# Optimization experiments

Measured on AMD Instinct MI355X. Metric: run time of the kernel, lower is better.

## Reference

```python
import jax, jax.numpy as jnp
import numpy as np

V, E, HD, NT = 50001, 256, 512, 24   # vocab, embed_dim, hidden_dim, tag_size
H = HD // 2                          # per-direction LSTM hidden
B, S = 64, 512


def setup_inputs() -> dict:
    key = jax.random.key(0)
    ks = jax.random.split(key, 18)
    lw = lambda k, sh, s=0.05: (jax.random.normal(k, sh, jnp.float32) * s)
    x = jax.random.randint(ks[0], (B, S), 0, V).astype(jnp.int32)
    lengths = jax.random.randint(ks[1], (B,), S // 2, S + 1)
    mask = jnp.arange(S)[None, :] < lengths[:, None]  # [B,S] bool, mask[:,0]=True
    return {
        "x": x,
        "mask": mask,
        "emb": lw(ks[2], (V, E), 0.1),
        "Wih_f": lw(ks[3], (4 * H, E)), "Whh_f": lw(ks[4], (4 * H, H)),
        "bih_f": lw(ks[5], (4 * H,)), "bhh_f": lw(ks[6], (4 * H,)),
        "Wih_b": lw(ks[7], (4 * H, E)), "Whh_b": lw(ks[8], (4 * H, H)),
        "bih_b": lw(ks[9], (4 * H,)), "bhh_b": lw(ks[10], (4 * H,)),
        "Wout": lw(ks[11], (NT, HD)), "bout": lw(ks[12], (NT,)),
        "trans": lw(ks[13], (NT, NT), 0.1),
        "start": lw(ks[14], (NT,), 0.1),
        "end": lw(ks[15], (NT,), 0.1),
    }


def _lstm_dir(xs, Wih, Whh, bih, bhh):
    # xs: [S, B, E] -> hs: [S, B, H]; torch gate order i, f, g, o
    Bn = xs.shape[1]
    h0 = jnp.zeros((Bn, H), xs.dtype)

    def step(carry, xt):
        h, c = carry
        g = xt @ Wih.T + h @ Whh.T + bih + bhh
        i, f, gg, o = jnp.split(g, 4, axis=-1)
        c = jax.nn.sigmoid(f) * c + jax.nn.sigmoid(i) * jnp.tanh(gg)
        h = jax.nn.sigmoid(o) * jnp.tanh(c)
        return (h, c), h

    _, hs = jax.lax.scan(step, (h0, h0), xs)
    return hs


def _viterbi(emissions, mask, trans, start, end):
    # emissions: [B, S, T]; mask: [B, S] bool. Returns (tags [B,S] int, best_score [B]).
    em = emissions.transpose(1, 0, 2)   # [S, B, T]
    mk = mask.transpose(1, 0)           # [S, B]
    nT = trans.shape[0]
    idx_id = jnp.arange(nT)[None, :]    # identity backpointers for padded steps
    score = start[None, :] + em[0]      # [B, T]

    def step(score, inp):
        e_t, m_t = inp
        cand = score[:, :, None] + trans[None, :, :] + e_t[:, None, :]  # [B,Tprev,Tnext]
        idx = jnp.argmax(cand, axis=1)
        best = jnp.max(cand, axis=1)
        idx = jnp.where(m_t[:, None], idx, idx_id)
        new_score = jnp.where(m_t[:, None], best, score)
        return new_score, idx

    score, hist = jax.lax.scan(step, score, (em[1:], mk[1:]))  # hist: [S-1, B, T]
    final = score + end[None, :]
    last_tag = jnp.argmax(final, axis=1)   # [B]
    best_score = jnp.max(final, axis=1)    # [B]

    def back(tag, h_t):
        prev = jnp.take_along_axis(h_t, tag[:, None], axis=1)[:, 0]
        return prev, tag

    tag0, ys = jax.lax.scan(back, last_tag, hist, reverse=True)
    tags = jnp.concatenate([tag0[None, :], ys], axis=0).T  # [B, S]
    return tags, best_score


def reference(x, mask, emb, Wih_f, Whh_f, bih_f, bhh_f, Wih_b, Whh_b, bih_b, bhh_b,
              Wout, bout, trans, start, end):
    e = emb[x]                      # [B, S, E] embedding gather
    xs = e.transpose(1, 0, 2)       # [S, B, E] time-major for scan
    hf = _lstm_dir(xs, Wih_f, Whh_f, bih_f, bhh_f)
    hb = jnp.flip(_lstm_dir(jnp.flip(xs, 0), Wih_b, Whh_b, bih_b, bhh_b), 0)
    h = jnp.concatenate([hf, hb], axis=-1)          # [S, B, HD]
    emis = (h @ Wout.T + bout).transpose(1, 0, 2)   # [B, S, T]
    tags, _ = _viterbi(emis, mask, trans, start, end)
    return tags
```

## Files before the change

### kernel.cpp

```cpp
#include <hip/hip_runtime.h>
#include <math.h>

#define B_   64
#define S_   512
#define E_   256
#define H_   256
#define G4H_ 1024
#define NT_  24

static const size_t HBUF_OFF  = 0;
static const size_t CST_OFF   = 131072;
static const size_t WHI_OFF   = 163840;
static const size_t WLO_OFF   = 425984;
static const size_t EMF_OFF   = 688128;
static const size_t EMB_OFF   = 1474560;
static const size_t HOUT_OFF  = 2260992;

typedef short  bf16x8_ __attribute__((ext_vector_type(8)));
typedef float  f32x4_  __attribute__((ext_vector_type(4)));

__device__ __forceinline__ float sigmoidf_(float x) {
  return 1.0f / (1.0f + expf(-x));
}

__device__ __forceinline__ unsigned short bf16_rne_(float v) {
  unsigned u = __float_as_uint(v);
  unsigned r = u + 0x7fffu + ((u >> 16) & 1u);
  return (unsigned short)(r >> 16);
}

__global__ __launch_bounds__(256) void k0_wconv(
    const float* __restrict__ Wf, const float* __restrict__ Wb,
    unsigned short* __restrict__ whi, unsigned short* __restrict__ wlo)
{
  int idx = blockIdx.x * 256 + threadIdx.x;
  int d   = idx >> 16;
  int i4  = idx & 65535;
  const float* W = d ? Wb : Wf;
  float4 v = *(const float4*)(W + (size_t)i4 * 4);
  float vv[4] = {v.x, v.y, v.z, v.w};
  unsigned short h[4], l[4];
#pragma unroll
  for (int e = 0; e < 4; ++e) {
    h[e] = bf16_rne_(vv[e]);
    float hf = __uint_as_float((unsigned)h[e] << 16);
    l[e] = bf16_rne_(vv[e] - hf);
  }
  size_t o = (size_t)d * 262144 + (size_t)i4 * 4;
  whi[o + 0] = h[0]; whi[o + 1] = h[1]; whi[o + 2] = h[2]; whi[o + 3] = h[3];
  wlo[o + 0] = l[0]; wlo[o + 1] = l[1]; wlo[o + 2] = l[2]; wlo[o + 3] = l[3];
}

__global__ __launch_bounds__(256) void k1_xpre_mfma(
    const int* __restrict__ x, const float* __restrict__ emb,
    const unsigned short* __restrict__ whi,
    const unsigned short* __restrict__ wlo,
    const float* __restrict__ bih_f, const float* __restrict__ bhh_f,
    const float* __restrict__ bih_b, const float* __restrict__ bhh_b,
    float* __restrict__ xpre_c, int chunk, int tc)
{
  __shared__ unsigned short Ahi[128][40], Alo[128][40];
  __shared__ unsigned short Bhi[128][40], Blo[128][40];
  __shared__ int xt[128];

  const int tid = threadIdx.x;
  const int wg  = blockIdx.x;
  const int per_dir = 4 * tc;
  const int d   = wg / per_dir;
  const int rem = wg % per_dir;
  const int m0  = (rem >> 3) * 128;
  const int n0  = (rem & 7) * 128;
  const int t0  = chunk * tc;

  const float* bih = d ? bih_b : bih_f;
  const float* bhh = d ? bhh_b : bhh_f;
  const unsigned short* Whi = whi + (size_t)d * 262144;
  const unsigned short* Wlo = wlo + (size_t)d * 262144;

  if (tid < 128) {
    int m = m0 + tid;
    int lt = m >> 6, b = m & 63;
    int tok = d ? (S_ - 1 - (t0 + lt)) : (t0 + lt);
    xt[tid] = x[b * S_ + tok];
  }

  const int lane = tid & 63, wid = tid >> 6;
  const int wr = wid >> 1, wc = wid & 1;
  const int fr = lane & 15, fq = lane >> 4;
  const int sr = tid >> 1, sh = tid & 1;

  f32x4_ acc[4][4];
#pragma unroll
  for (int i = 0; i < 4; ++i)
#pragma unroll
    for (int j = 0; j < 4; ++j) acc[i][j] = (f32x4_){0.f, 0.f, 0.f, 0.f};

  for (int slab = 0; slab < 8; ++slab) {
    const int k0 = slab * 32;
    __syncthreads();
    {
      const float* src = emb + (size_t)xt[sr] * E_ + k0 + sh * 16;
      unsigned short h[16], l[16];
#pragma unroll
      for (int q = 0; q < 4; ++q) {
        float4 v = *(const float4*)(src + q * 4);
        float vv[4] = {v.x, v.y, v.z, v.w};
#pragma unroll
        for (int e = 0; e < 4; ++e) {
          h[q * 4 + e] = bf16_rne_(vv[e]);
          float hf = __uint_as_float((unsigned)h[q * 4 + e] << 16);
          l[q * 4 + e] = bf16_rne_(vv[e] - hf);
        }
      }
      *(bf16x8_*)&Ahi[sr][sh * 16 + 0] = *(bf16x8_*)&h[0];
      *(bf16x8_*)&Ahi[sr][sh * 16 + 8] = *(bf16x8_*)&h[8];
      *(bf16x8_*)&Alo[sr][sh * 16 + 0] = *(bf16x8_*)&l[0];
      *(bf16x8_*)&Alo[sr][sh * 16 + 8] = *(bf16x8_*)&l[8];
    }
    {
      const size_t o = (size_t)(n0 + sr) * E_ + k0 + sh * 16;
      *(bf16x8_*)&Bhi[sr][sh * 16 + 0] = *(const bf16x8_*)(Whi + o);
      *(bf16x8_*)&Bhi[sr][sh * 16 + 8] = *(const bf16x8_*)(Whi + o + 8);
      *(bf16x8_*)&Blo[sr][sh * 16 + 0] = *(const bf16x8_*)(Wlo + o);
      *(bf16x8_*)&Blo[sr][sh * 16 + 8] = *(const bf16x8_*)(Wlo + o + 8);
    }
    __syncthreads();

    bf16x8_ ah[4], al[4], bh[4], bl[4];
#pragma unroll
    for (int mi = 0; mi < 4; ++mi) {
      int row = 64 * wr + mi * 16 + fr;
      ah[mi] = *(bf16x8_*)&Ahi[row][fq * 8];
      al[mi] = *(bf16x8_*)&Alo[row][fq * 8];
    }
#pragma unroll
    for (int ni = 0; ni < 4; ++ni) {
      int row = 64 * wc + ni * 16 + fr;
      bh[ni] = *(bf16x8_*)&Bhi[row][fq * 8];
      bl[ni] = *(bf16x8_*)&Blo[row][fq * 8];
    }
#pragma unroll
    for (int mi = 0; mi < 4; ++mi)
#pragma unroll
      for (int ni = 0; ni < 4; ++ni) {
        acc[mi][ni] = __builtin_amdgcn_mfma_f32_16x16x32_bf16(
            al[mi], bl[ni], acc[mi][ni], 0, 0, 0);
        acc[mi][ni] = __builtin_amdgcn_mfma_f32_16x16x32_bf16(
            al[mi], bh[ni], acc[mi][ni], 0, 0, 0);
        acc[mi][ni] = __builtin_amdgcn_mfma_f32_16x16x32_bf16(
            ah[mi], bl[ni], acc[mi][ni], 0, 0, 0);
        acc[mi][ni] = __builtin_amdgcn_mfma_f32_16x16x32_bf16(
            ah[mi], bh[ni], acc[mi][ni], 0, 0, 0);
      }
  }

  float bias[4];
#pragma unroll
  for (int ni = 0; ni < 4; ++ni) {
    int col = n0 + 64 * wc + ni * 16 + fr;
    bias[ni] = bih[col] + bhh[col];
  }
  const size_t base = (size_t)(d * tc * 64) * G4H_;
#pragma unroll
  for (int mi = 0; mi < 4; ++mi)
#pragma unroll
    for (int ni = 0; ni < 4; ++ni) {
      int col = n0 + 64 * wc + ni * 16 + fr;
#pragma unroll
      for (int r = 0; r < 4; ++r) {
        int m = m0 + 64 * wr + mi * 16 + fq * 4 + r;
        xpre_c[base + (size_t)m * G4H_ + col] = acc[mi][ni][r] + bias[ni];
      }
    }
}

__global__ __launch_bounds__(256, 1) void k2_lstm(
    const float* __restrict__ Whh_f, const float* __restrict__ Whh_b,
    const float* __restrict__ xpre_c, float* __restrict__ hout_c,
    unsigned long long* hbuf, float* cstate, int chunk, int tc)
{
  __shared__ float hTb[16][260];
  __shared__ float part[2][4][16][36];

  const int tid = threadIdx.x;
  const int wg  = blockIdx.x;
  const int d   = wg >> 7;
  const int bg  = (wg >> 5) & 3;
  const int s   = wg & 31;
  const int b0  = bg * 16;
  const float* Whh = d ? Whh_b : Whh_f;

  const int w     = tid >> 6;
  const int lane  = tid & 63;
  const int bl16  = lane & 15;
  const int kb    = lane >> 4;
  const int kbase = w * 64 + kb * 16;
  const int ks    = tid >> 5;
  const int tl    = tid & 31, bt = tl & 3, rt = tl >> 2;
  const int pbl   = tid >> 3, pj = tid & 7;

  float wreg[4][32];
#pragma unroll
  for (int ri = 0; ri < 4; ++ri) {
    int r = rt * 4 + ri, g = r >> 3, j = r & 7;
    const float* src = Whh + ((size_t)(g * H_ + s * 8 + j)) * H_ + ks * 32;
#pragma unroll
    for (int q = 0; q < 8; ++q) {
      float4 v = *(const float4*)(src + q * 4);
      wreg[ri][q * 4 + 0] = v.x; wreg[ri][q * 4 + 1] = v.y;
      wreg[ri][q * 4 + 2] = v.z; wreg[ri][q * 4 + 3] = v.w;
    }
  }

  float c_reg = 0.0f;
  if (chunk > 0 && tid < 128)
    c_reg = cstate[((size_t)d * B_ + b0 + pbl) * H_ + s * 8 + pj];

  for (int tt = 1; tt <= tc; ++tt) {
    const int t  = chunk * tc + tt;
    const int lt = tt - 1;
    const int p  = tt & 1;

    float xp[4];
    if (tid < 128) {
#pragma unroll
      for (int g = 0; g < 4; ++g)
        xp[g] = xpre_c[((size_t)(d * tc + lt) * B_ + b0 + pbl) * G4H_ +
                       g * H_ + s * 8 + pj];
    }

    {
      const unsigned expt = (unsigned)(t - 1);
      const unsigned long long* hb =
          hbuf + ((size_t)(((t - 1) & 1) * 2 + d)) * (256 * 64);
      const size_t a0 = (size_t)kbase * 64 + b0 + bl16;
      unsigned long long e[16];
#pragma unroll
      for (int i = 0; i < 16; ++i)
        e[i] = __hip_atomic_load(hb + a0 + (size_t)i * 64,
                                 __ATOMIC_RELAXED, __HIP_MEMORY_SCOPE_AGENT);
      int lim = 0;
      while (true) {
        unsigned bad = 0;
#pragma unroll
        for (int i = 0; i < 16; ++i)
          if ((unsigned)(e[i] >> 32) != expt) bad |= (1u << i);
        if (bad == 0) break;
        if (++lim > (1 << 18)) break;
#pragma unroll
        for (int i = 0; i < 16; ++i)
          if (bad & (1u << i))
            e[i] = __hip_atomic_load(hb + a0 + (size_t)i * 64,
                                     __ATOMIC_RELAXED,
                                     __HIP_MEMORY_SCOPE_AGENT);
      }
      float4 v0, v1, v2, v3;
      v0.x = __uint_as_float((unsigned)e[0]);  v0.y = __uint_as_float((unsigned)e[1]);
      v0.z = __uint_as_float((unsigned)e[2]);  v0.w = __uint_as_float((unsigned)e[3]);
      v1.x = __uint_as_float((unsigned)e[4]);  v1.y = __uint_as_float((unsigned)e[5]);
      v1.z = __uint_as_float((unsigned)e[6]);  v1.w = __uint_as_float((unsigned)e[7]);
      v2.x = __uint_as_float((unsigned)e[8]);  v2.y = __uint_as_float((unsigned)e[9]);
      v2.z = __uint_as_float((unsigned)e[10]); v2.w = __uint_as_float((unsigned)e[11]);
      v3.x = __uint_as_float((unsigned)e[12]); v3.y = __uint_as_float((unsigned)e[13]);
      v3.z = __uint_as_float((unsigned)e[14]); v3.w = __uint_as_float((unsigned)e[15]);
      *(float4*)&hTb[bl16][kbase +  0] = v0;
      *(float4*)&hTb[bl16][kbase +  4] = v1;
      *(float4*)&hTb[bl16][kbase +  8] = v2;
      *(float4*)&hTb[bl16][kbase + 12] = v3;
    }

    float acc[4][4];
#pragma unroll
    for (int bi = 0; bi < 4; ++bi)
#pragma unroll
      for (int ri = 0; ri < 4; ++ri) acc[bi][ri] = 0.0f;
#pragma unroll
    for (int kq = 0; kq < 8; ++kq) {
      const int k0 = ks * 32 + kq * 4;
      float4 h4[4];
#pragma unroll
      for (int bi = 0; bi < 4; ++bi)
        h4[bi] = *(float4*)&hTb[bt * 4 + bi][k0];
#pragma unroll
      for (int kk = 0; kk < 4; ++kk) {
#pragma unroll
        for (int bi = 0; bi < 4; ++bi) {
          const float hv = kk == 0 ? h4[bi].x : kk == 1 ? h4[bi].y
                         : kk == 2 ? h4[bi].z : h4[bi].w;
#pragma unroll
          for (int ri = 0; ri < 4; ++ri)
            acc[bi][ri] = fmaf(hv, wreg[ri][kq * 4 + kk], acc[bi][ri]);
        }
      }
    }
#pragma unroll
    for (int bi = 0; bi < 4; ++bi)
#pragma unroll
      for (int ri = 0; ri < 4; ++ri)
        acc[bi][ri] += __shfl_xor(acc[bi][ri], 32, 64);
    if (lane < 32) {
#pragma unroll
      for (int bi = 0; bi < 4; ++bi) {
        float4 v = make_float4(acc[bi][0], acc[bi][1], acc[bi][2], acc[bi][3]);
        *(float4*)&part[p][w][bt * 4 + bi][rt * 4] = v;
      }
    }
    __syncthreads();

    if (tid < 128) {
      const int bglob = b0 + pbl;
      float gsum[4];
#pragma unroll
      for (int g = 0; g < 4; ++g) {
        const int r = g * 8 + pj;
        gsum[g] = xp[g] + ((part[p][0][pbl][r] + part[p][1][pbl][r]) +
                           (part[p][2][pbl][r] + part[p][3][pbl][r]));
      }
      float si = sigmoidf_(gsum[0]);
      float sf = sigmoidf_(gsum[1]);
      float tg = tanhf(gsum[2]);
      float so = sigmoidf_(gsum[3]);
      c_reg = sf * c_reg + si * tg;
      float h = so * tanhf(c_reg);
      unsigned long long pk =
          (((unsigned long long)(unsigned)t) << 32) |
          (unsigned long long)__float_as_uint(h);
      __hip_atomic_store(hbuf + ((size_t)((t & 1) * 2 + d)) * (256 * 64) +
                             (size_t)(s * 8 + pj) * 64 + bglob,
                         pk, __ATOMIC_RELAXED, __HIP_MEMORY_SCOPE_AGENT);
      hout_c[((size_t)(d * tc + lt) * B_ + bglob) * H_ + s * 8 + pj] = h;
    }
  }

  if (tid < 128)
    cstate[((size_t)d * B_ + b0 + pbl) * H_ + s * 8 + pj] = c_reg;
}

__global__ __launch_bounds__(256) void k3_emis(
    const float* __restrict__ hout_c, const float* __restrict__ Wout,
    float* __restrict__ emisF, float* __restrict__ emisB, int chunk, int tc)
{
  __shared__ float hh[8][264];
  const int tid = threadIdx.x;
  const int nt8 = tc >> 3;
  const int per_d = 64 * nt8;
  const int d   = blockIdx.x / per_d;
  const int rem = blockIdx.x % per_d;
  const int b   = rem / nt8;
  const int lt0 = (rem % nt8) * 8;
  float* emisX = d ? emisB : emisF;
  {
    int r = tid >> 5, q = tid & 31;
    const float* src = hout_c + ((size_t)(d * tc + lt0 + r) * B_ + b) * H_;
#pragma unroll
    for (int i = 0; i < 2; ++i) {
      int f4i = q + 32 * i;
      *(float4*)&hh[r][f4i * 4] = *(const float4*)(src + f4i * 4);
    }
  }
  __syncthreads();
  if (tid < 192) {
    int r = tid / 24, tag = tid % 24;
    float acc = 0.0f;
    const float* w = Wout + (size_t)tag * 512 + d * 256;
#pragma unroll 4
    for (int k4 = 0; k4 < 64; ++k4) {
      float4 wv = *(const float4*)(w + k4 * 4);
      float4 hv = *(const float4*)&hh[r][k4 * 4];
      acc = fmaf(wv.x, hv.x, acc);
      acc = fmaf(wv.y, hv.y, acc);
      acc = fmaf(wv.z, hv.z, acc);
      acc = fmaf(wv.w, hv.w, acc);
    }
    int lt = lt0 + r;
    int tok = d ? (S_ - 1 - (chunk * tc + lt)) : (chunk * tc + lt);
    emisX[((size_t)b * S_ + tok) * NT_ + tag] = acc;
  }
}

__global__ __launch_bounds__(64) void k4_viterbi(
    const float* __restrict__ emisF, const float* __restrict__ emisB,
    const float* __restrict__ bout, const unsigned char* __restrict__ mb,
    const float* __restrict__ trans, const float* __restrict__ startv,
    const float* __restrict__ endv, int* __restrict__ outp)
{
  __shared__ float tl[24 * 25];
  __shared__ float sc[24];
  __shared__ float fin[24];
  __shared__ unsigned char hist[511 * 24];
  const int b = blockIdx.x;
  const int tid = threadIdx.x;
  const int is_bool = mb[1];

  for (int i = tid; i < 576; i += 64) tl[(i / 24) * 25 + (i % 24)] = trans[i];
  if (tid < 24) {
    size_t e0 = (size_t)b * S_ * NT_ + tid;
    sc[tid] = startv[tid] + (emisF[e0] + emisB[e0] + bout[tid]);
  }
  __syncthreads();

  for (int t = 1; t < S_; ++t) {
    float best = -3.4e38f, scj = 0.f;
    int idx = 0;
    int m;
    {
      int mi = b * S_ + t;
      m = is_bool ? (int)mb[mi] : (int)mb[mi << 2];
    }
    if (tid < 24) {
      size_t ei = ((size_t)b * S_ + t) * NT_ + tid;
      float e = emisF[ei] + emisB[ei] + bout[tid];
      for (int i = 0; i < 24; ++i) {
        float v = (sc[i] + tl[i * 25 + tid]) + e;
        if (v > best) { best = v; idx = i; }
      }
      scj = sc[tid];
    }
    __syncthreads();
    if (tid < 24) {
      sc[tid] = m ? best : scj;
      hist[(t - 1) * 24 + tid] = (unsigned char)(m ? idx : tid);
    }
    __syncthreads();
  }
  if (tid < 24) fin[tid] = sc[tid] + endv[tid];
  __syncthreads();
  if (tid == 0) {
    int tag = 0; float best = fin[0];
    for (int i = 1; i < 24; ++i)
      if (fin[i] > best) { best = fin[i]; tag = i; }
    outp[b * S_ + (S_ - 1)] = tag;
    for (int tt = S_ - 2; tt >= 0; --tt) {
      tag = hist[tt * 24 + tag];
      outp[b * S_ + tt] = tag;
    }
  }
}

extern "C" void kernel_launch(void* const* d_in, const int* in_sizes, int n_in,
                              void* d_out, int out_size, void* d_ws,
                              size_t ws_size, hipStream_t stream)
{
  const int*   x      = (const int*)d_in[0];
  const unsigned char* maskb = (const unsigned char*)d_in[1];
  const float* emb    = (const float*)d_in[2];
  const float* Wih_f  = (const float*)d_in[3];
  const float* Whh_f  = (const float*)d_in[4];
  const float* bih_f  = (const float*)d_in[5];
  const float* bhh_f  = (const float*)d_in[6];
  const float* Wih_b  = (const float*)d_in[7];
  const float* Whh_b  = (const float*)d_in[8];
  const float* bih_b  = (const float*)d_in[9];
  const float* bhh_b  = (const float*)d_in[10];
  const float* Wout   = (const float*)d_in[11];
  const float* bout   = (const float*)d_in[12];
  const float* trans  = (const float*)d_in[13];
  const float* startv = (const float*)d_in[14];
  const float* endv   = (const float*)d_in[15];

  int tc = 8;
  {
    const int cand[6] = {512, 256, 128, 64, 32, 16};
    for (int i = 0; i < 6; ++i) {
      size_t needF = HOUT_OFF + (size_t)cand[i] * (2 * B_ * H_ + 2 * B_ * G4H_);
      if (needF * sizeof(float) <= ws_size) { tc = cand[i]; break; }
    }
  }
  const int nc = S_ / tc;

  float* ws     = (float*)d_ws;
  unsigned long long* hbuf = (unsigned long long*)(ws + HBUF_OFF);
  float* cstate = ws + CST_OFF;
  unsigned short* whi = (unsigned short*)(ws + WHI_OFF);
  unsigned short* wlo = (unsigned short*)(ws + WLO_OFF);
  float* emisF  = ws + EMF_OFF;
  float* emisB  = ws + EMB_OFF;
  float* hout_c = ws + HOUT_OFF;
  float* xpre_c = hout_c + (size_t)tc * 2 * B_ * H_;

  hipMemsetAsync(d_ws, 0, 131072 * sizeof(float), stream);
  hipLaunchKernelGGL(k0_wconv, dim3(512), dim3(256), 0, stream,
                     Wih_f, Wih_b, whi, wlo);

  for (int c = 0; c < nc; ++c) {
    hipLaunchKernelGGL(k1_xpre_mfma, dim3(8 * tc), dim3(256), 0, stream,
                       x, emb, whi, wlo, bih_f, bhh_f, bih_b, bhh_b,
                       xpre_c, c, tc);
    hipLaunchKernelGGL(k2_lstm, dim3(256), dim3(256), 0, stream,
                       Whh_f, Whh_b, xpre_c, hout_c, hbuf, cstate, c, tc);
    hipLaunchKernelGGL(k3_emis, dim3(2 * 64 * (tc / 8)), dim3(256), 0, stream,
                       hout_c, Wout, emisF, emisB, c, tc);
  }
  hipLaunchKernelGGL(k4_viterbi, dim3(64), dim3(64), 0, stream,
                     emisF, emisB, bout, maskb, trans, startv, endv,
                     (int*)d_out);
}
```

Baseline: 2.660 ms.

## Retile LSTM recurrent matvec per thread and preload Viterbi emissions into LDS

The recurrent LSTM kernel now gives each thread 8 batch rows by 4 gate rows over a 16-wide k slice instead of 4x4 over 32. This halves the weight registers and adds a second cross-lane shuffle reduction. The h tile rows are permuted so each thread's batch rows interleave, to reduce LDS bank conflicts. The Viterbi kernel stages the summed forward and backward emissions and the mask into shared memory up front, which takes global-memory latency out of the serial 511-step loop at the cost of about 49KB of extra LDS per block.

```diff
diff --git a/kernel.cpp b/kernel.cpp
--- a/kernel.cpp
+++ b/kernel.cpp
@@ -195,17 +195,19 @@
   const int bl16  = lane & 15;
   const int kb    = lane >> 4;
   const int kbase = w * 64 + kb * 16;
-  const int ks    = tid >> 5;
-  const int tl    = tid & 31, bt = tl & 3, rt = tl >> 2;
+  const int prow  = ((bl16 & 7) << 1) | (bl16 >> 3);
+  const int ksc16 = (tid >> 4) * 16;
+  const int rt    = (tid >> 1) & 7;
+  const int bt    = tid & 1;
   const int pbl   = tid >> 3, pj = tid & 7;
 
-  float wreg[4][32];
+  float wreg[4][16];
 #pragma unroll
   for (int ri = 0; ri < 4; ++ri) {
     int r = rt * 4 + ri, g = r >> 3, j = r & 7;
-    const float* src = Whh + ((size_t)(g * H_ + s * 8 + j)) * H_ + ks * 32;
-#pragma unroll
-    for (int q = 0; q < 8; ++q) {
+    const float* src = Whh + ((size_t)(g * H_ + s * 8 + j)) * H_ + ksc16;
+#pragma unroll
+    for (int q = 0; q < 4; ++q) {
       float4 v = *(const float4*)(src + q * 4);
       wreg[ri][q * 4 + 0] = v.x; wreg[ri][q * 4 + 1] = v.y;
       wreg[ri][q * 4 + 2] = v.z; wreg[ri][q * 4 + 3] = v.w;
@@ -263,28 +265,28 @@
       v2.z = __uint_as_float((unsigned)e[10]); v2.w = __uint_as_float((unsigned)e[11]);
       v3.x = __uint_as_float((unsigned)e[12]); v3.y = __uint_as_float((unsigned)e[13]);
       v3.z = __uint_as_float((unsigned)e[14]); v3.w = __uint_as_float((unsigned)e[15]);
-      *(float4*)&hTb[bl16][kbase +  0] = v0;
-      *(float4*)&hTb[bl16][kbase +  4] = v1;
-      *(float4*)&hTb[bl16][kbase +  8] = v2;
-      *(float4*)&hTb[bl16][kbase + 12] = v3;
-    }
-
-    float acc[4][4];
-#pragma unroll
-    for (int bi = 0; bi < 4; ++bi)
+      *(float4*)&hTb[prow][kbase +  0] = v0;
+      *(float4*)&hTb[prow][kbase +  4] = v1;
+      *(float4*)&hTb[prow][kbase +  8] = v2;
+      *(float4*)&hTb[prow][kbase + 12] = v3;
+    }
+
+    float acc[8][4];
+#pragma unroll
+    for (int bi = 0; bi < 8; ++bi)
 #pragma unroll
       for (int ri = 0; ri < 4; ++ri) acc[bi][ri] = 0.0f;
 #pragma unroll
-    for (int kq = 0; kq < 8; ++kq) {
-      const int k0 = ks * 32 + kq * 4;
-      float4 h4[4];
-#pragma unroll
-      for (int bi = 0; bi < 4; ++bi)
-        h4[bi] = *(float4*)&hTb[bt * 4 + bi][k0];
+    for (int kq = 0; kq < 4; ++kq) {
+      const int k0 = ksc16 + kq * 4;
+      float4 h4[8];
+#pragma unroll
+      for (int bi = 0; bi < 8; ++bi)
+        h4[bi] = *(float4*)&hTb[(bi << 1) | bt][k0];
 #pragma unroll
       for (int kk = 0; kk < 4; ++kk) {
 #pragma unroll
-        for (int bi = 0; bi < 4; ++bi) {
+        for (int bi = 0; bi < 8; ++bi) {
           const float hv = kk == 0 ? h4[bi].x : kk == 1 ? h4[bi].y
                          : kk == 2 ? h4[bi].z : h4[bi].w;
 #pragma unroll
@@ -294,15 +296,17 @@
       }
     }
 #pragma unroll
-    for (int bi = 0; bi < 4; ++bi)
-#pragma unroll
-      for (int ri = 0; ri < 4; ++ri)
+    for (int bi = 0; bi < 8; ++bi)
+#pragma unroll
+      for (int ri = 0; ri < 4; ++ri) {
+        acc[bi][ri] += __shfl_xor(acc[bi][ri], 16, 64);
         acc[bi][ri] += __shfl_xor(acc[bi][ri], 32, 64);
-    if (lane < 32) {
-#pragma unroll
-      for (int bi = 0; bi < 4; ++bi) {
+      }
+    if ((lane & 48) == 0) {
+#pragma unroll
+      for (int bi = 0; bi < 8; ++bi) {
         float4 v = make_float4(acc[bi][0], acc[bi][1], acc[bi][2], acc[bi][3]);
-        *(float4*)&part[p][w][bt * 4 + bi][rt * 4] = v;
+        *(float4*)&part[p][w][bt * 8 + bi][rt * 4] = v;
       }
     }
     __syncthreads();
@@ -385,6 +389,8 @@
     const float* __restrict__ endv, int* __restrict__ outp)
 {
   __shared__ float tl[24 * 25];
+  __shared__ __align__(16) float et[512][24];
+  __shared__ unsigned char mk[512];
   __shared__ float sc[24];
   __shared__ float fin[24];
   __shared__ unsigned char hist[511 * 24];
@@ -393,23 +399,31 @@
   const int is_bool = mb[1];
 
   for (int i = tid; i < 576; i += 64) tl[(i / 24) * 25 + (i % 24)] = trans[i];
-  if (tid < 24) {
-    size_t e0 = (size_t)b * S_ * NT_ + tid;
-    sc[tid] = startv[tid] + (emisF[e0] + emisB[e0] + bout[tid]);
-  }
+  for (int t = tid; t < S_; t += 64) {
+    int mi = b * S_ + t;
+    mk[t] = is_bool ? mb[mi] : mb[mi << 2];
+  }
+  {
+    const float4* eF = (const float4*)(emisF + (size_t)b * S_ * NT_);
+    const float4* eB = (const float4*)(emisB + (size_t)b * S_ * NT_);
+    float4* ed = (float4*)&et[0][0];
+    for (int i = tid; i < (S_ * NT_) / 4; i += 64) {
+      float4 a = eF[i], c = eB[i];
+      ed[i] = make_float4(a.x + c.x, a.y + c.y, a.z + c.z, a.w + c.w);
+    }
+  }
+  const float boutr = (tid < 24) ? bout[tid] : 0.0f;
+  __syncthreads();
+
+  if (tid < 24) sc[tid] = startv[tid] + (et[0][tid] + boutr);
   __syncthreads();
 
   for (int t = 1; t < S_; ++t) {
     float best = -3.4e38f, scj = 0.f;
     int idx = 0;
-    int m;
-    {
-      int mi = b * S_ + t;
-      m = is_bool ? (int)mb[mi] : (int)mb[mi << 2];
-    }
+    const int m = mk[t];
     if (tid < 24) {
-      size_t ei = ((size_t)b * S_ + t) * NT_ + tid;
-      float e = emisF[ei] + emisB[ei] + bout[tid];
+      float e = et[t][tid] + boutr;
       for (int i = 0; i < 24; ++i) {
         float v = (sc[i] + tl[i * 25 + tid]) + e;
         if (v > best) { best = v; idx = i; }
```

After: 2.907 ms. +9.3%, slower.

## Replace per-element tagged h exchange with per-block flags; stage Viterbi emissions in LDS

Applied to the files above, without the earlier changes.

The LSTM recurrence previously packed each h value with a timestep tag into 64-bit words and spun on all of them. It now stores plain floats in a batch-major buffer, and each workgroup raises a release flag after a block barrier. Consumers spin on 32 flags with a wave ballot, then read h with contiguous 64-bit loads. This cuts the polling traffic and the exchanged bytes, at the cost of an extra __syncthreads and a relaxed-acquire ordering subtlety. The Viterbi kernel also preloads the summed emissions and the mask into shared memory, so the serial loop no longer reads global memory.

```diff
diff --git a/kernel.cpp b/kernel.cpp
--- a/kernel.cpp
+++ b/kernel.cpp
@@ -9,6 +9,7 @@
 #define NT_  24
 
 static const size_t HBUF_OFF  = 0;
+static const size_t FLG_OFF   = 65536;
 static const size_t CST_OFF   = 131072;
 static const size_t WHI_OFF   = 163840;
 static const size_t WLO_OFF   = 425984;
@@ -177,7 +178,7 @@
 __global__ __launch_bounds__(256, 1) void k2_lstm(
     const float* __restrict__ Whh_f, const float* __restrict__ Whh_b,
     const float* __restrict__ xpre_c, float* __restrict__ hout_c,
-    unsigned long long* hbuf, float* cstate, int chunk, int tc)
+    float* hbuf2, unsigned* flags, float* cstate, int chunk, int tc)
 {
   __shared__ float hTb[16][260];
   __shared__ float part[2][4][16][36];
@@ -193,8 +194,7 @@
   const int w     = tid >> 6;
   const int lane  = tid & 63;
   const int bl16  = lane & 15;
-  const int kb    = lane >> 4;
-  const int kbase = w * 64 + kb * 16;
+  const int kg    = w * 4 + (lane >> 4);
   const int ks    = tid >> 5;
   const int tl    = tid & 31, bt = tl & 3, rt = tl >> 2;
   const int pbl   = tid >> 3, pj = tid & 7;
@@ -231,42 +231,39 @@
 
     {
       const unsigned expt = (unsigned)(t - 1);
-      const unsigned long long* hb =
-          hbuf + ((size_t)(((t - 1) & 1) * 2 + d)) * (256 * 64);
-      const size_t a0 = (size_t)kbase * 64 + b0 + bl16;
-      unsigned long long e[16];
-#pragma unroll
-      for (int i = 0; i < 16; ++i)
-        e[i] = __hip_atomic_load(hb + a0 + (size_t)i * 64,
-                                 __ATOMIC_RELAXED, __HIP_MEMORY_SCOPE_AGENT);
+      const unsigned* fl =
+          flags + (size_t)((((t - 1) & 1) * 2 + d) * 4 + bg) * 32;
+      unsigned v = expt;
+      if (lane < 32)
+        v = __hip_atomic_load(fl + lane, __ATOMIC_RELAXED,
+                              __HIP_MEMORY_SCOPE_AGENT);
       int lim = 0;
-      while (true) {
-        unsigned bad = 0;
-#pragma unroll
-        for (int i = 0; i < 16; ++i)
-          if ((unsigned)(e[i] >> 32) != expt) bad |= (1u << i);
-        if (bad == 0) break;
-        if (++lim > (1 << 18)) break;
-#pragma unroll
-        for (int i = 0; i < 16; ++i)
-          if (bad & (1u << i))
-            e[i] = __hip_atomic_load(hb + a0 + (size_t)i * 64,
-                                     __ATOMIC_RELAXED,
-                                     __HIP_MEMORY_SCOPE_AGENT);
-      }
-      float4 v0, v1, v2, v3;
-      v0.x = __uint_as_float((unsigned)e[0]);  v0.y = __uint_as_float((unsigned)e[1]);
-      v0.z = __uint_as_float((unsigned)e[2]);  v0.w = __uint_as_float((unsigned)e[3]);
-      v1.x = __uint_as_float((unsigned)e[4]);  v1.y = __uint_as_float((unsigned)e[5]);
-      v1.z = __uint_as_float((unsigned)e[6]);  v1.w = __uint_as_float((unsigned)e[7]);
-      v2.x = __uint_as_float((unsigned)e[8]);  v2.y = __uint_as_float((unsigned)e[9]);
-      v2.z = __uint_as_float((unsigned)e[10]); v2.w = __uint_as_float((unsigned)e[11]);
-      v3.x = __uint_as_float((unsigned)e[12]); v3.y = __uint_as_float((unsigned)e[13]);
-      v3.z = __uint_as_float((unsigned)e[14]); v3.w = __uint_as_float((unsigned)e[15]);
-      *(float4*)&hTb[bl16][kbase +  0] = v0;
-      *(float4*)&hTb[bl16][kbase +  4] = v1;
-      *(float4*)&hTb[bl16][kbase +  8] = v2;
-      *(float4*)&hTb[bl16][kbase + 12] = v3;
+      while (__ballot(v != expt)) {
+        if (++lim > (1 << 20)) break;
+        if (v != expt)
+          v = __hip_atomic_load(fl + lane, __ATOMIC_RELAXED,
+                                __HIP_MEMORY_SCOPE_AGENT);
+      }
+    }
+
+    {
+      const unsigned long long* hb = (const unsigned long long*)
+          (hbuf2 + (size_t)(((t - 1) & 1) * 2 + d) * (64 * 256));
+      const size_t a0 = ((size_t)(b0 + bl16) * 256 + kg * 16) >> 1;
+      unsigned long long e[8];
+#pragma unroll
+      for (int i = 0; i < 8; ++i)
+        e[i] = __hip_atomic_load(hb + a0 + i, __ATOMIC_RELAXED,
+                                 __HIP_MEMORY_SCOPE_AGENT);
+#pragma unroll
+      for (int q = 0; q < 4; ++q) {
+        float4 v;
+        v.x = __uint_as_float((unsigned)e[2 * q]);
+        v.y = __uint_as_float((unsigned)(e[2 * q] >> 32));
+        v.z = __uint_as_float((unsigned)e[2 * q + 1]);
+        v.w = __uint_as_float((unsigned)(e[2 * q + 1] >> 32));
+        *(float4*)&hTb[bl16][kg * 16 + q * 4] = v;
+      }
     }
 
     float acc[4][4];
@@ -322,14 +319,16 @@
       float so = sigmoidf_(gsum[3]);
       c_reg = sf * c_reg + si * tg;
       float h = so * tanhf(c_reg);
-      unsigned long long pk =
-          (((unsigned long long)(unsigned)t) << 32) |
-          (unsigned long long)__float_as_uint(h);
-      __hip_atomic_store(hbuf + ((size_t)((t & 1) * 2 + d)) * (256 * 64) +
-                             (size_t)(s * 8 + pj) * 64 + bglob,
-                         pk, __ATOMIC_RELAXED, __HIP_MEMORY_SCOPE_AGENT);
+      __hip_atomic_store(hbuf2 + (size_t)((t & 1) * 2 + d) * (64 * 256) +
+                             (size_t)bglob * 256 + s * 8 + pj,
+                         h, __ATOMIC_RELAXED, __HIP_MEMORY_SCOPE_AGENT);
       hout_c[((size_t)(d * tc + lt) * B_ + bglob) * H_ + s * 8 + pj] = h;
     }
+    __syncthreads();
+    if (tid == 0)
+      __hip_atomic_store(
+          flags + (size_t)(((t & 1) * 2 + d) * 4 + bg) * 32 + s,
+          (unsigned)t, __ATOMIC_RELEASE, __HIP_MEMORY_SCOPE_AGENT);
   }
 
   if (tid < 128)
@@ -385,6 +384,8 @@
     const float* __restrict__ endv, int* __restrict__ outp)
 {
   __shared__ float tl[24 * 25];
+  __shared__ __align__(16) float et[512][24];
+  __shared__ unsigned char mk[512];
   __shared__ float sc[24];
   __shared__ float fin[24];
   __shared__ unsigned char hist[511 * 24];
@@ -393,23 +394,31 @@
   const int is_bool = mb[1];
 
   for (int i = tid; i < 576; i += 64) tl[(i / 24) * 25 + (i % 24)] = trans[i];
-  if (tid < 24) {
-    size_t e0 = (size_t)b * S_ * NT_ + tid;
-    sc[tid] = startv[tid] + (emisF[e0] + emisB[e0] + bout[tid]);
-  }
+  for (int t = tid; t < S_; t += 64) {
+    int mi = b * S_ + t;
+    mk[t] = is_bool ? mb[mi] : mb[mi << 2];
+  }
+  {
+    const float4* eF = (const float4*)(emisF + (size_t)b * S_ * NT_);
+    const float4* eB = (const float4*)(emisB + (size_t)b * S_ * NT_);
+    float4* ed = (float4*)&et[0][0];
+    for (int i = tid; i < (S_ * NT_) / 4; i += 64) {
+      float4 a = eF[i], c = eB[i];
+      ed[i] = make_float4(a.x + c.x, a.y + c.y, a.z + c.z, a.w + c.w);
+    }
+  }
+  const float boutr = (tid < 24) ? bout[tid] : 0.0f;
+  __syncthreads();
+
+  if (tid < 24) sc[tid] = startv[tid] + (et[0][tid] + boutr);
   __syncthreads();
 
   for (int t = 1; t < S_; ++t) {
     float best = -3.4e38f, scj = 0.f;
     int idx = 0;
-    int m;
-    {
-      int mi = b * S_ + t;
-      m = is_bool ? (int)mb[mi] : (int)mb[mi << 2];
-    }
+    const int m = mk[t];
     if (tid < 24) {
-      size_t ei = ((size_t)b * S_ + t) * NT_ + tid;
-      float e = emisF[ei] + emisB[ei] + bout[tid];
+      float e = et[t][tid] + boutr;
       for (int i = 0; i < 24; ++i) {
         float v = (sc[i] + tl[i * 25 + tid]) + e;
         if (v > best) { best = v; idx = i; }
@@ -469,7 +478,8 @@
   const int nc = S_ / tc;
 
   float* ws     = (float*)d_ws;
-  unsigned long long* hbuf = (unsigned long long*)(ws + HBUF_OFF);
+  float* hbuf2  = ws + HBUF_OFF;
+  unsigned* flags = (unsigned*)(ws + FLG_OFF);
   float* cstate = ws + CST_OFF;
   unsigned short* whi = (unsigned short*)(ws + WHI_OFF);
   unsigned short* wlo = (unsigned short*)(ws + WLO_OFF);
@@ -487,7 +497,8 @@
                        x, emb, whi, wlo, bih_f, bhh_f, bih_b, bhh_b,
                        xpre_c, c, tc);
     hipLaunchKernelGGL(k2_lstm, dim3(256), dim3(256), 0, stream,
-                       Whh_f, Whh_b, xpre_c, hout_c, hbuf, cstate, c, tc);
+                       Whh_f, Whh_b, xpre_c, hout_c, hbuf2, flags, cstate,
+                       c, tc);
     hipLaunchKernelGGL(k3_emis, dim3(2 * 64 * (tc / 8)), dim3(256), 0, stream,
                        hout_c, Wout, emisF, emisB, c, tc);
   }
```

Result: slower. 6.900 ms (+159.4%).
